# Optimization experiments

Hardware: AMD Instinct MI355X
Metric: run time of the kernel (lower is better)

The kernel has to match this reference:

```python
import jax, jax.numpy as jnp
import numpy as np

D_MODEL = 2048
HEADDIM = 32
NHEADS = D_MODEL // HEADDIM  # 64
BLOCK = 256
EPS = 1e-4


def segsum(x):
    # x: (..., T) -> (..., T, T) stable segment sums, -inf above diagonal
    T = x.shape[-1]
    xe = jnp.broadcast_to(x[..., None], x.shape + (T,))  # (..., d, e)
    lower = jnp.tril(jnp.ones((T, T), dtype=bool), -1)
    xe = jnp.where(lower, xe, 0.0)
    s = jnp.cumsum(xe, axis=-2)
    incl = jnp.tril(jnp.ones((T, T), dtype=bool), 0)
    return jnp.where(incl, s, -jnp.inf)


def ssd_minimal_discrete(X, A, B, C, block_len):
    # X: (b, L, h, p); A: (b, L, h); B, C: (b, L, h, n). L % block_len == 0.
    b, Lm, h, p = X.shape
    c = Lm // block_len
    Xb = X.reshape(b, c, block_len, h, p)
    Bb = B.reshape(b, c, block_len, h, B.shape[-1])
    Cb = C.reshape(b, c, block_len, h, C.shape[-1])
    Ab = A.reshape(b, c, block_len, h).transpose(0, 3, 1, 2)  # (b, h, c, l)
    A_cumsum = jnp.cumsum(Ab, axis=-1)
    Lmat = jnp.exp(segsum(Ab))  # (b, h, c, l, s)
    # 1. intra-chunk (diagonal block) output
    Y_diag = jnp.einsum('bclhn,bcshn,bhcls,bcshp->bclhp', Cb, Bb, Lmat, Xb)
    # 2. per-chunk states
    decay_states = jnp.exp(A_cumsum[:, :, :, -1:] - A_cumsum)  # (b, h, c, l)
    states = jnp.einsum('bclhn,bhcl,bclhp->bchpn', Bb, decay_states, Xb)
    # 3. inter-chunk recurrence
    init = jnp.zeros_like(states[:, :1])
    states = jnp.concatenate([init, states], axis=1)  # (b, c+1, h, p, n)
    A_last = jnp.pad(A_cumsum[:, :, :, -1], ((0, 0), (0, 0), (1, 0)))  # (b, h, c+1)
    decay_chunk = jnp.exp(segsum(A_last))  # (b, h, c+1, c+1)
    new_states = jnp.einsum('bhzc,bchpn->bzhpn', decay_chunk, states)
    states_in, final_state = new_states[:, :-1], new_states[:, -1]
    # 4. state -> output within chunks
    state_decay_out = jnp.exp(A_cumsum)  # (b, h, c, l)
    Y_off = jnp.einsum('bclhn,bchpn,bhcl->bclhp', Cb, states_in, state_decay_out)
    Y = (Y_diag + Y_off).reshape(b, Lm, h, p)
    return Y, final_state


def setup_inputs() -> dict:
    key = jax.random.key(0)
    k1, k2 = jax.random.split(key)
    Bsz, Lfull, M = 2, 4096, 2048
    hidden_states = jax.random.normal(k1, (Bsz, M, D_MODEL), dtype=jnp.float32)
    # boundaries at even positions: exactly M boundaries per row, position 0 is a boundary
    boundary_mask = jnp.broadcast_to((jnp.arange(Lfull) % 2 == 0)[None, :], (Bsz, Lfull))
    boundary_prob = jax.random.uniform(k2, (Bsz, Lfull, 2), dtype=jnp.float32)
    mask = jnp.ones((Bsz, Lfull), dtype=bool)
    return {"hidden_states": hidden_states, "boundary_mask": boundary_mask,
            "boundary_prob": boundary_prob, "mask": mask}


def reference(hidden_states, boundary_mask, boundary_prob, mask):
    Bsz, Lfull = boundary_mask.shape
    M = hidden_states.shape[1]
    # select boundary-position probabilities, in order, first M
    p = jnp.clip(boundary_prob[..., -1].astype(jnp.float32), EPS, 1.0 - EPS)
    token_idx = jnp.arange(Lfull)[None, :] + (~boundary_mask).astype(jnp.int32) * Lfull
    order = jnp.argsort(token_idx, axis=1, stable=True)
    p_sel = jnp.take_along_axis(p, order[:, :M], axis=1)  # (B, M)
    dt = jnp.log(1.0 / (1.0 - p_sel))
    x = hidden_states.astype(jnp.float32) / dt[..., None]
    Xr = x.reshape(Bsz, M, NHEADS, HEADDIM)
    A_dt = -jnp.broadcast_to(dt[:, :, None], (Bsz, M, NHEADS))  # A = -1, A*dt
    B_ssd = jnp.broadcast_to(p_sel[:, :, None, None], (Bsz, M, NHEADS, 1))
    C_ssd = jnp.ones_like(B_ssd)
    out, _ = ssd_minimal_discrete(Xr, A_dt, B_ssd, C_ssd, BLOCK)
    out = out.reshape(Bsz, M, D_MODEL)
    # plug back: each uncompressed token reads the EMA value of its chunk
    plug = jnp.cumsum(boundary_mask.astype(jnp.int32), axis=1) - 1  # (B, L)
    out = jnp.take_along_axis(out, plug[:, :, None], axis=1)  # (B, L, d_model)
    return out
```

## Files before the change

### kernel.cpp

```cpp
#include <hip/hip_runtime.h>
#include <math.h>

#define BSZ    2
#define LFULL  4096
#define MLEN   2048
#define DMODEL 2048
#define CLIP_EPS 1e-4f
#define CCH    256
#define TCH    8

typedef float f4 __attribute__((ext_vector_type(4)));

__global__ __launch_bounds__(256) void k1_prep(
    const int* __restrict__ bmask_raw, const float* __restrict__ bprob,
    int* __restrict__ Ls, int* __restrict__ Le,
    float* __restrict__ wA, float* __restrict__ eA,
    float* __restrict__ cde, float* __restrict__ Pc)
{
  const int b   = blockIdx.x;
  const int tid = threadIdx.x;

  __shared__ int   s_cnt[257];
  __shared__ int   s_mode;
  __shared__ int   s_ntrue;
  __shared__ int   s_sel[MLEN];
  __shared__ float s_e[MLEN];

  if (tid == 0) {
    unsigned w0 = ((const unsigned*)bmask_raw)[0];
    s_mode = (w0 <= 1u) ? 1 : 0;
  }
  __syncthreads();
  const int mode = s_mode;
  const unsigned char* bmask_u8 = (const unsigned char*)bmask_raw;

  const int PER = LFULL / 256;
  const int base = tid * PER;

  int cnt = 0;
  for (int i = 0; i < PER; ++i) {
    const int L = base + i;
    const int v = mode ? (bmask_raw[b * LFULL + L] != 0)
                       : (bmask_u8[b * LFULL + L] != 0);
    cnt += v;
  }
  s_cnt[tid] = cnt;
  __syncthreads();

  if (tid < 64) {
    const int j = tid * 4;
    const int c0 = s_cnt[j], c1 = s_cnt[j + 1], c2 = s_cnt[j + 2], c3 = s_cnt[j + 3];
    const int mysum = c0 + c1 + c2 + c3;
    int incl = mysum;
    #pragma unroll
    for (int off = 1; off < 64; off <<= 1) {
      const int v = __shfl_up(incl, off, 64);
      if (tid >= off) incl += v;
    }
    const int excl = incl - mysum;
    s_cnt[j]     = excl;
    s_cnt[j + 1] = excl + c0;
    s_cnt[j + 2] = excl + c0 + c1;
    s_cnt[j + 3] = excl + c0 + c1 + c2;
    if (tid == 63) { s_cnt[256] = incl; s_ntrue = incl; }
  }
  __syncthreads();
  const int ntrue = s_ntrue;

  int trun = s_cnt[tid];
  for (int i = 0; i < PER; ++i) {
    const int L = base + i;
    const int v = mode ? (bmask_raw[b * LFULL + L] != 0)
                       : (bmask_u8[b * LFULL + L] != 0);
    if (v) {
      if (trun < MLEN) s_sel[trun] = L;
      ++trun;
    } else {
      const int f = L - trun;
      const int slot = ntrue + f;
      if (slot < MLEN) s_sel[slot] = L;
    }
  }
  __syncthreads();

  for (int j = tid; j < MLEN; j += 256) {
    const int L = s_sel[j];
    float p = bprob[((size_t)b * LFULL + L) * 2 + 1];
    p = fminf(fmaxf(p, CLIP_EPS), 1.0f - CLIP_EPS);
    const float dt = -log1pf(-p);
    wA[b * MLEN + j] = p / dt;
    const float e = 1.0f - p;
    eA[b * MLEN + j] = e;
    s_e[j] = e;
  }
  __syncthreads();

  {
    const int c = tid;
    const int o = c * TCH;
    float run = 1.0f;
    #pragma unroll
    for (int i = 0; i < TCH; ++i) {
      run *= s_e[o + i];
      cde[b * MLEN + o + i] = run;
    }
    Pc[b * CCH + c] = run;
  }

  const int nb = (ntrue < MLEN) ? ntrue : MLEN;
  for (int j = tid; j < MLEN; j += 256) {
    int ls, le;
    if (nb == 0) {
      ls = (j == 0) ? 0 : LFULL;
      le = (j == 0) ? LFULL : LFULL;
    } else if (j < nb) {
      ls = (j == 0) ? 0 : s_sel[j];
      le = (j == nb - 1) ? LFULL : s_sel[j + 1];
    } else {
      ls = LFULL; le = LFULL;
    }
    Ls[b * MLEN + j] = ls;
    Le[b * MLEN + j] = le;
  }
}

__global__ __launch_bounds__(1024, 4) void k2b_fused(
    const float* __restrict__ hid, const float* __restrict__ wA,
    const float* __restrict__ eA, const float* __restrict__ cde,
    const float* __restrict__ Pc,
    const int* __restrict__ Ls, const int* __restrict__ Le,
    float* __restrict__ out)
{
  const int tid = threadIdx.x;
  const int j   = tid & 3;
  const int c   = tid >> 2;
  const int bx  = blockIdx.x;
  const int b   = blockIdx.y;

  __shared__ float sP[CCH];
  __shared__ f4    sS[CCH][4];

  const int d4 = bx * 4 + j;
  const int o  = b * MLEN + c * TCH;

  const f4* xp = (const f4*)hid + ((size_t)o * DMODEL >> 2) + d4;
  f4 xr[TCH];
  f4 st = {0.f, 0.f, 0.f, 0.f};
  #pragma unroll
  for (int t = 0; t < TCH; ++t) {
    const f4 x = xp[(size_t)t * (DMODEL / 4)];
    const float w = wA[o + t], e = eA[o + t];
    st.x = fmaf(e, st.x, w * x.x);
    st.y = fmaf(e, st.y, w * x.y);
    st.z = fmaf(e, st.z, w * x.z);
    st.w = fmaf(e, st.w, w * x.w);
    xr[t] = st;
  }
  sS[c][j] = st;
  if (j == 0) sP[c] = Pc[b * CCH + c];
  __syncthreads();

  for (int dstep = 1; dstep < CCH; dstep <<= 1) {
    const float pc = sP[c];
    float pd = 1.0f;
    f4 sd = {0.f, 0.f, 0.f, 0.f};
    if (c >= dstep) { pd = sP[c - dstep]; sd = sS[c - dstep][j]; }
    __syncthreads();
    if (c >= dstep) {
      f4 cur = sS[c][j];
      cur.x = fmaf(pc, sd.x, cur.x);
      cur.y = fmaf(pc, sd.y, cur.y);
      cur.z = fmaf(pc, sd.z, cur.z);
      cur.w = fmaf(pc, sd.w, cur.w);
      sS[c][j] = cur;
      if (j == 0) sP[c] = pc * pd;
    }
    __syncthreads();
  }

  f4 H = {0.f, 0.f, 0.f, 0.f};
  if (c > 0) H = sS[c - 1][j];

  f4* op = (f4*)out + ((size_t)b * LFULL * DMODEL >> 2) + d4;
  #pragma unroll
  for (int t = 0; t < TCH; ++t) {
    const float cd = cde[o + t];
    f4 y;
    y.x = fmaf(cd, H.x, xr[t].x);
    y.y = fmaf(cd, H.y, xr[t].y);
    y.z = fmaf(cd, H.z, xr[t].z);
    y.w = fmaf(cd, H.w, xr[t].w);
    const int ls = Ls[o + t], le = Le[o + t];
    for (int L = ls; L < le; ++L) {
      __builtin_nontemporal_store(y, op + (size_t)L * (DMODEL / 4));
    }
  }
}

extern "C" void kernel_launch(void* const* d_in, const int* in_sizes, int n_in,
                              void* d_out, int out_size, void* d_ws, size_t ws_size,
                              hipStream_t stream) {
  const float* hid   = (const float*)d_in[0];
  const int*   bmask = (const int*)d_in[1];
  const float* bprob = (const float*)d_in[2];
  float*       out   = (float*)d_out;

  char* ws = (char*)d_ws;
  const size_t SZI = (size_t)BSZ * MLEN * sizeof(int);
  const size_t SZF = (size_t)BSZ * MLEN * sizeof(float);
  int*   Ls  = (int*)(ws);
  int*   Le  = (int*)(ws + SZI);
  float* wA  = (float*)(ws + 2 * SZI);
  float* eA  = (float*)(ws + 2 * SZI + SZF);
  float* cde = (float*)(ws + 2 * SZI + 2 * SZF);
  float* Pc  = (float*)(ws + 2 * SZI + 3 * SZF);

  k1_prep<<<dim3(BSZ), dim3(256), 0, stream>>>(bmask, bprob, Ls, Le, wA, eA, cde, Pc);

  k2b_fused<<<dim3(DMODEL / 16, BSZ), dim3(1024), 0, stream>>>(
      hid, wA, eA, cde, Pc, Ls, Le, out);
}
```

Measured before the change: 118.6 us.

## Fuse prep kernel into main scan kernel, recomputing boundary selection per block

```diff
diff --git a/kernel.cpp b/kernel.cpp
--- a/kernel.cpp
+++ b/kernel.cpp
@@ -11,45 +11,54 @@
 
 typedef float f4 __attribute__((ext_vector_type(4)));
 
-__global__ __launch_bounds__(256) void k1_prep(
-    const int* __restrict__ bmask_raw, const float* __restrict__ bprob,
-    int* __restrict__ Ls, int* __restrict__ Le,
-    float* __restrict__ wA, float* __restrict__ eA,
-    float* __restrict__ cde, float* __restrict__ Pc)
+__global__ __launch_bounds__(1024, 2) void mega(
+    const float* __restrict__ hid, const int* __restrict__ bmask_raw,
+    const float* __restrict__ bprob, float* __restrict__ out)
 {
-  const int b   = blockIdx.x;
   const int tid = threadIdx.x;
+  const int j   = tid & 3;
+  const int c   = tid >> 2;
+  const int bx  = blockIdx.x;
+  const int b   = blockIdx.y;
 
-  __shared__ int   s_cnt[257];
-  __shared__ int   s_mode;
-  __shared__ int   s_ntrue;
-  __shared__ int   s_sel[MLEN];
-  __shared__ float s_e[MLEN];
+  __shared__ union {
+    struct { int cnt[257]; int mode; int ntrue; int sel[MLEN]; } k1;
+    struct { float P[CCH]; f4 S[CCH][4]; } scan;
+  } sm;
+
+  const int d4 = bx * 4 + j;
+  const int o  = b * MLEN + c * TCH;
+  const f4* xp = (const f4*)hid + ((size_t)o * DMODEL >> 2) + d4;
+  f4 xr[TCH];
+  #pragma unroll
+  for (int t = 0; t < TCH; ++t) xr[t] = xp[(size_t)t * (DMODEL / 4)];
 
   if (tid == 0) {
     unsigned w0 = ((const unsigned*)bmask_raw)[0];
-    s_mode = (w0 <= 1u) ? 1 : 0;
+    sm.k1.mode = (w0 <= 1u) ? 1 : 0;
   }
   __syncthreads();
-  const int mode = s_mode;
+  const int mode = sm.k1.mode;
   const unsigned char* bmask_u8 = (const unsigned char*)bmask_raw;
 
   const int PER = LFULL / 256;
-  const int base = tid * PER;
-
-  int cnt = 0;
-  for (int i = 0; i < PER; ++i) {
-    const int L = base + i;
-    const int v = mode ? (bmask_raw[b * LFULL + L] != 0)
-                       : (bmask_u8[b * LFULL + L] != 0);
-    cnt += v;
+  if (tid < 256) {
+    const int base = tid * PER;
+    int cnt = 0;
+    for (int i = 0; i < PER; ++i) {
+      const int L = base + i;
+      const int v = mode ? (bmask_raw[b * LFULL + L] != 0)
+                         : (bmask_u8[b * LFULL + L] != 0);
+      cnt += v;
+    }
+    sm.k1.cnt[tid] = cnt;
   }
-  s_cnt[tid] = cnt;
   __syncthreads();
 
   if (tid < 64) {
-    const int j = tid * 4;
-    const int c0 = s_cnt[j], c1 = s_cnt[j + 1], c2 = s_cnt[j + 2], c3 = s_cnt[j + 3];
+    const int q = tid * 4;
+    const int c0 = sm.k1.cnt[q], c1 = sm.k1.cnt[q + 1];
+    const int c2 = sm.k1.cnt[q + 2], c3 = sm.k1.cnt[q + 3];
     const int mysum = c0 + c1 + c2 + c3;
     int incl = mysum;
     #pragma unroll
@@ -58,140 +67,107 @@
       if (tid >= off) incl += v;
     }
     const int excl = incl - mysum;
-    s_cnt[j]     = excl;
-    s_cnt[j + 1] = excl + c0;
-    s_cnt[j + 2] = excl + c0 + c1;
-    s_cnt[j + 3] = excl + c0 + c1 + c2;
-    if (tid == 63) { s_cnt[256] = incl; s_ntrue = incl; }
+    sm.k1.cnt[q]     = excl;
+    sm.k1.cnt[q + 1] = excl + c0;
+    sm.k1.cnt[q + 2] = excl + c0 + c1;
+    sm.k1.cnt[q + 3] = excl + c0 + c1 + c2;
+    if (tid == 63) { sm.k1.cnt[256] = incl; sm.k1.ntrue = incl; }
   }
   __syncthreads();
-  const int ntrue = s_ntrue;
+  const int ntrue = sm.k1.ntrue;
 
-  int trun = s_cnt[tid];
-  for (int i = 0; i < PER; ++i) {
-    const int L = base + i;
-    const int v = mode ? (bmask_raw[b * LFULL + L] != 0)
-                       : (bmask_u8[b * LFULL + L] != 0);
-    if (v) {
-      if (trun < MLEN) s_sel[trun] = L;
-      ++trun;
-    } else {
-      const int f = L - trun;
-      const int slot = ntrue + f;
-      if (slot < MLEN) s_sel[slot] = L;
+  if (tid < 256) {
+    const int base = tid * PER;
+    int trun = sm.k1.cnt[tid];
+    for (int i = 0; i < PER; ++i) {
+      const int L = base + i;
+      const int v = mode ? (bmask_raw[b * LFULL + L] != 0)
+                         : (bmask_u8[b * LFULL + L] != 0);
+      if (v) {
+        if (trun < MLEN) sm.k1.sel[trun] = L;
+        ++trun;
+      } else {
+        const int f = L - trun;
+        const int slot = ntrue + f;
+        if (slot < MLEN) sm.k1.sel[slot] = L;
+      }
     }
   }
   __syncthreads();
 
-  for (int j = tid; j < MLEN; j += 256) {
-    const int L = s_sel[j];
-    float p = bprob[((size_t)b * LFULL + L) * 2 + 1];
-    p = fminf(fmaxf(p, CLIP_EPS), 1.0f - CLIP_EPS);
-    const float dt = -log1pf(-p);
-    wA[b * MLEN + j] = p / dt;
-    const float e = 1.0f - p;
-    eA[b * MLEN + j] = e;
-    s_e[j] = e;
+  const int nb = (ntrue < MLEN) ? ntrue : MLEN;
+  float w[TCH], e[TCH], cd[TCH];
+  int   ls[TCH], le[TCH];
+  {
+    float run = 1.0f;
+    #pragma unroll
+    for (int t = 0; t < TCH; ++t) {
+      const int g = c * TCH + t;
+      const int L = sm.k1.sel[g];
+      float p = bprob[((size_t)b * LFULL + L) * 2 + 1];
+      p = fminf(fmaxf(p, CLIP_EPS), 1.0f - CLIP_EPS);
+      const float dt = -log1pf(-p);
+      w[t] = p / dt;
+      e[t] = 1.0f - p;
+      run *= e[t];
+      cd[t] = run;
+      if (nb == 0) {
+        ls[t] = (g == 0) ? 0 : LFULL;
+        le[t] = (g == 0) ? LFULL : LFULL;
+      } else if (g < nb) {
+        ls[t] = (g == 0) ? 0 : sm.k1.sel[g];
+        le[t] = (g == nb - 1) ? LFULL : sm.k1.sel[g + 1];
+      } else {
+        ls[t] = LFULL; le[t] = LFULL;
+      }
+    }
   }
   __syncthreads();
 
-  {
-    const int c = tid;
-    const int o = c * TCH;
-    float run = 1.0f;
-    #pragma unroll
-    for (int i = 0; i < TCH; ++i) {
-      run *= s_e[o + i];
-      cde[b * MLEN + o + i] = run;
-    }
-    Pc[b * CCH + c] = run;
-  }
-
-  const int nb = (ntrue < MLEN) ? ntrue : MLEN;
-  for (int j = tid; j < MLEN; j += 256) {
-    int ls, le;
-    if (nb == 0) {
-      ls = (j == 0) ? 0 : LFULL;
-      le = (j == 0) ? LFULL : LFULL;
-    } else if (j < nb) {
-      ls = (j == 0) ? 0 : s_sel[j];
-      le = (j == nb - 1) ? LFULL : s_sel[j + 1];
-    } else {
-      ls = LFULL; le = LFULL;
-    }
-    Ls[b * MLEN + j] = ls;
-    Le[b * MLEN + j] = le;
-  }
-}
-
-__global__ __launch_bounds__(1024, 4) void k2b_fused(
-    const float* __restrict__ hid, const float* __restrict__ wA,
-    const float* __restrict__ eA, const float* __restrict__ cde,
-    const float* __restrict__ Pc,
-    const int* __restrict__ Ls, const int* __restrict__ Le,
-    float* __restrict__ out)
-{
-  const int tid = threadIdx.x;
-  const int j   = tid & 3;
-  const int c   = tid >> 2;
-  const int bx  = blockIdx.x;
-  const int b   = blockIdx.y;
-
-  __shared__ float sP[CCH];
-  __shared__ f4    sS[CCH][4];
-
-  const int d4 = bx * 4 + j;
-  const int o  = b * MLEN + c * TCH;
-
-  const f4* xp = (const f4*)hid + ((size_t)o * DMODEL >> 2) + d4;
-  f4 xr[TCH];
   f4 st = {0.f, 0.f, 0.f, 0.f};
   #pragma unroll
   for (int t = 0; t < TCH; ++t) {
-    const f4 x = xp[(size_t)t * (DMODEL / 4)];
-    const float w = wA[o + t], e = eA[o + t];
-    st.x = fmaf(e, st.x, w * x.x);
-    st.y = fmaf(e, st.y, w * x.y);
-    st.z = fmaf(e, st.z, w * x.z);
-    st.w = fmaf(e, st.w, w * x.w);
+    const f4 x = xr[t];
+    st.x = fmaf(e[t], st.x, w[t] * x.x);
+    st.y = fmaf(e[t], st.y, w[t] * x.y);
+    st.z = fmaf(e[t], st.z, w[t] * x.z);
+    st.w = fmaf(e[t], st.w, w[t] * x.w);
     xr[t] = st;
   }
-  sS[c][j] = st;
-  if (j == 0) sP[c] = Pc[b * CCH + c];
+  sm.scan.S[c][j] = st;
+  if (j == 0) sm.scan.P[c] = cd[TCH - 1];
   __syncthreads();
 
   for (int dstep = 1; dstep < CCH; dstep <<= 1) {
-    const float pc = sP[c];
+    const float pc = sm.scan.P[c];
     float pd = 1.0f;
     f4 sd = {0.f, 0.f, 0.f, 0.f};
-    if (c >= dstep) { pd = sP[c - dstep]; sd = sS[c - dstep][j]; }
+    if (c >= dstep) { pd = sm.scan.P[c - dstep]; sd = sm.scan.S[c - dstep][j]; }
     __syncthreads();
     if (c >= dstep) {
-      f4 cur = sS[c][j];
+      f4 cur = sm.scan.S[c][j];
       cur.x = fmaf(pc, sd.x, cur.x);
       cur.y = fmaf(pc, sd.y, cur.y);
       cur.z = fmaf(pc, sd.z, cur.z);
       cur.w = fmaf(pc, sd.w, cur.w);
-      sS[c][j] = cur;
-      if (j == 0) sP[c] = pc * pd;
+      sm.scan.S[c][j] = cur;
+      if (j == 0) sm.scan.P[c] = pc * pd;
     }
     __syncthreads();
   }
 
   f4 H = {0.f, 0.f, 0.f, 0.f};
-  if (c > 0) H = sS[c - 1][j];
+  if (c > 0) H = sm.scan.S[c - 1][j];
 
   f4* op = (f4*)out + ((size_t)b * LFULL * DMODEL >> 2) + d4;
   #pragma unroll
   for (int t = 0; t < TCH; ++t) {
-    const float cd = cde[o + t];
     f4 y;
-    y.x = fmaf(cd, H.x, xr[t].x);
-    y.y = fmaf(cd, H.y, xr[t].y);
-    y.z = fmaf(cd, H.z, xr[t].z);
-    y.w = fmaf(cd, H.w, xr[t].w);
-    const int ls = Ls[o + t], le = Le[o + t];
-    for (int L = ls; L < le; ++L) {
+    y.x = fmaf(cd[t], H.x, xr[t].x);
+    y.y = fmaf(cd[t], H.y, xr[t].y);
+    y.z = fmaf(cd[t], H.z, xr[t].z);
+    y.w = fmaf(cd[t], H.w, xr[t].w);
+    for (int L = ls[t]; L < le[t]; ++L) {
       __builtin_nontemporal_store(y, op + (size_t)L * (DMODEL / 4));
     }
   }
@@ -204,19 +180,7 @@
   const int*   bmask = (const int*)d_in[1];
   const float* bprob = (const float*)d_in[2];
   float*       out   = (float*)d_out;
+  (void)d_ws; (void)ws_size;
 
-  char* ws = (char*)d_ws;
-  const size_t SZI = (size_t)BSZ * MLEN * sizeof(int);
-  const size_t SZF = (size_t)BSZ * MLEN * sizeof(float);
-  int*   Ls  = (int*)(ws);
-  int*   Le  = (int*)(ws + SZI);
-  float* wA  = (float*)(ws + 2 * SZI);
-  float* eA  = (float*)(ws + 2 * SZI + SZF);
-  float* cde = (float*)(ws + 2 * SZI + 2 * SZF);
-  float* Pc  = (float*)(ws + 2 * SZI + 3 * SZF);
-
-  k1_prep<<<dim3(BSZ), dim3(256), 0, stream>>>(bmask, bprob, Ls, Le, wA, eA, cde, Pc);
-
-  k2b_fused<<<dim3(DMODEL / 16, BSZ), dim3(1024), 0, stream>>>(
-      hid, wA, eA, cde, Pc, Ls, Le, out);
+  mega<<<dim3(DMODEL / 16, BSZ), dim3(1024), 0, stream>>>(hid, bmask, bprob, out);
 }
```

After: 119.0 us. About the same (+0.4%).
